# Optimization experiments

Measured on AMD Instinct MI355X. Metric: run time of the kernel, lower is better.

The kernel has to match this reference:

```python
import jax, jax.numpy as jnp
import numpy as np
from jax import lax

# pywt db4 filters. REC_LO is pywt's rec_lo; the others follow pywt's QMF relations:
# rec_hi[k] = (-1)**k * rec_lo[F-1-k]; dec_lo = rec_lo[::-1]; dec_hi = rec_hi[::-1].
REC_LO = np.array([0.23037781330885523, 0.7148465705525415, 0.6308807679295904,
                   -0.027983769416983849, -0.18703481171888114, 0.030841381835986965,
                   0.032883011666982945, -0.010597401784997278], dtype=np.float32)
F = 8
REC_HI = np.array([(-1.0) ** k * REC_LO[F - 1 - k] for k in range(F)], dtype=np.float32)
DEC_LO = REC_LO[::-1].copy()
DEC_HI = REC_HI[::-1].copy()
LEVELS = 3


def _conv(x, kern, stride=1, lhs_dilation=1, padding=((0, 0),)):
    # x: (N, 1, L) ; 1-D correlation (jax conv does NOT flip the kernel)
    k = jnp.asarray(kern, x.dtype).reshape(1, 1, -1)
    return lax.conv_general_dilated(x, k, window_strides=(stride,), padding=padding,
                                    lhs_dilation=(lhs_dilation,),
                                    dimension_numbers=('NCH', 'OIH', 'NCH'))


def dwt(x):
    # pywt single-level dwt, mode='symmetric': extend by F-1 each side, then
    # decimated convolution with dec filters. Equivalent to: drop first extended
    # sample and stride-2 correlate with reversed dec filter (= rec filter).
    xe = jnp.pad(x, ((0, 0), (0, 0), (F - 1, F - 1)), mode='symmetric')[..., 1:]
    cA = _conv(xe, REC_LO, stride=2)   # rev(DEC_LO) == REC_LO
    cD = _conv(xe, REC_HI, stride=2)   # rev(DEC_HI) == REC_HI
    return cA, cD


def idwt(a, d):
    # pywt idwt: upsample by 2 (zeros between samples, len 2L-1), full-convolve
    # with rec filters, trim F-2 from each side -> len 2L - F + 2.
    # Via dilated conv: lhs_dilation=2, pad 1 each side, correlate with rev(rec)=dec.
    ra = _conv(a, DEC_LO, lhs_dilation=2, padding=((1, 1),))
    rd = _conv(d, DEC_HI, lhs_dilation=2, padding=((1, 1),))
    return ra + rd


def waverec(coeffs):
    a = coeffs[0]
    for d in coeffs[1:]:
        if a.shape[-1] == d.shape[-1] + 1:
            a = a[..., :-1]
        a = idwt(a, d)
    return a


def setup_inputs() -> dict:
    key = jax.random.key(0)
    x = jax.random.normal(key, (32, 64, 8192), dtype=jnp.float32)
    return {"x": x}


def reference(x):
    B, C, n = x.shape
    a = x.reshape(B * C, 1, n)
    details = []
    for _ in range(LEVELS):
        a, d = dwt(a)
        details.append(d)
    coeffs = [a] + details[::-1]  # [cA_L, cD_L, ..., cD_1] as in pywt.wavedec
    bands = []
    for i in range(LEVELS + 1):
        kept = [c if j == i else jnp.zeros_like(c) for j, c in enumerate(coeffs)]
        rec = waverec(kept)[..., :n]
        bands.append(rec.reshape(B, C, n))
    return tuple(bands)
```

## Files before the change

kernel.cpp:

```cpp
#include <hip/hip_runtime.h>


#define T      256
#define N0     8192
#define L1     4099
#define L2     2053
#define L3     1030
#define NROWS  2048
#define TW     256
#define WSLICE 960

#define RL0 0.23037781330885523f
#define RL1 0.7148465705525415f
#define RL2 0.6308807679295904f
#define RL3 (-0.02798376941698385f)
#define RL4 (-0.18703481171888114f)
#define RL5 0.030841381835986965f
#define RL6 0.032883011666982945f
#define RL7 (-0.010597401784997278f)

__device__ __forceinline__ int reflect(int m, int n)
{
    m = (m < 0) ? (-1 - m) : m;
    m = (m >= n) ? (2 * n - 1 - m) : m;
    return m;
}

__device__ __forceinline__ void fwd_win(const float* __restrict__ src, int src_lo,
                                        float* __restrict__ dstA, float* __restrict__ dstD,
                                        int out_lo, int out_len, int Lv, int lane)
{
    const float lo[8] = {RL0, RL1, RL2, RL3, RL4, RL5, RL6, RL7};
    const float hi[8] = {RL7, -RL6, RL5, -RL4, RL3, -RL2, RL1, -RL0};
    const float2* s2 = (const float2*)src;
    for (int idx = lane; idx < out_len; idx += 64) {
        int g  = out_lo + idx;
        int ge = reflect(g, Lv);
        int h  = (2 * ge - 6 - src_lo) >> 1;
        float2 p0 = s2[h], p1 = s2[h + 1], p2 = s2[h + 2], p3 = s2[h + 3];
        float w[8] = {p0.x, p0.y, p1.x, p1.y, p2.x, p2.y, p3.x, p3.y};
        float sa = 0.f, sd = 0.f;
#pragma unroll
        for (int k = 0; k < 8; ++k) {
            sa = fmaf(w[k], lo[k], sa);
            sd = fmaf(w[k], hi[k], sd);
        }
        dstA[idx] = sa;
        dstD[idx] = sd;
    }
}

__device__ __forceinline__ void up_win(const float* __restrict__ src, int src_lo,
                                       float* __restrict__ dst, int t0, int pairs,
                                       float o0, float o1, float o2, float o3,
                                       float e0, float e1, float e2, float e3, int lane)
{
    for (int idx = lane; idx < pairs; idx += 64) {
        int b = t0 + idx - src_lo;
        float s0 = src[b], s1 = src[b + 1], s2 = src[b + 2], s3 = src[b + 3];
        float ev = s0 * e0 + s1 * e1 + s2 * e2 + s3 * e3;
        float od = s0 * o0 + s1 * o1 + s2 * o2 + s3 * o3;
        ((float2*)dst)[idx] = make_float2(ev, od);
    }
}

__device__ __forceinline__ void fin_win(const float* __restrict__ src, int src_lo, int w0,
                                        float* __restrict__ g,
                                        float o0, float o1, float o2, float o3,
                                        float e0, float e1, float e2, float e3, int lane)
{
    int b = (w0 >> 1) + 2 * lane - src_lo;
    const float2* s2 = (const float2*)src;
    float2 q0 = s2[b >> 1], q1 = s2[(b >> 1) + 1];
    float s4 = src[b + 4];
    float a0 = q0.x, a1 = q0.y, a2 = q1.x, a3 = q1.y;
    float4 o;
    o.x = a0 * e0 + a1 * e1 + a2 * e2 + a3 * e3;
    o.y = a0 * o0 + a1 * o1 + a2 * o2 + a3 * o3;
    o.z = a1 * e0 + a2 * e1 + a3 * e2 + s4 * e3;
    o.w = a1 * o0 + a2 * o1 + a3 * o2 + s4 * o3;
    ((float4*)(g + w0))[lane] = o;
}


__global__ __launch_bounds__(T) void wavelet_bands(const float* __restrict__ x,
                                                   float* __restrict__ out)
{
    __shared__ float buf[4 * WSLICE];
    const int tid  = threadIdx.x;
    const int lane = tid & 63;
    const int wid  = tid >> 6;
    const int bid  = blockIdx.x;
    const int row  = bid >> 3;
    const int w0   = ((bid & 7) * 4 + wid) * TW;

    float* wbuf = buf + wid * WSLICE;
    float* xw  = wbuf;
    float* a1w = wbuf + 360;
    float* d1w = wbuf + 534;
    float* a2w = wbuf + 708;
    float* d2w = wbuf + 792;
    float* a3w = wbuf + 876;
    float* d3w = wbuf + 915;
    float* t2  = wbuf;
    float* t1a = wbuf + 136;
    float* t1d = wbuf + 208;
    float* t2a = wbuf + 360;
    float* t2d = wbuf + 534;

    const int lo1 = (w0 >> 1) - 18;
    const int lo2 = (w0 >> 2) - 6;
    const int lo3 = (w0 >> 3);
    const int lox = w0 - 48;

    const float* xr = x + (size_t)row * N0;
    const size_t band = (size_t)NROWS * N0;
    float* o0p = out + (size_t)row * N0;
    float* o1p = o0p + band;
    float* o2p = o0p + 2 * band;
    float* o3p = o0p + 3 * band;

    if (w0 == 0 || w0 == N0 - TW) {
        for (int idx = lane; idx < 360; idx += 64)
            xw[idx] = xr[reflect(lox + idx, N0)];
    } else {
        const float4* xr4 = (const float4*)xr;
        float4* xw4 = (float4*)xw;
        const int q0 = lox >> 2;
        for (int i = lane; i < 90; i += 64)
            xw4[i] = xr4[q0 + i];
    }

    fwd_win(xw, lox, a1w, d1w, lo1, TW / 2 + 46, L1, lane);

    fwd_win(a1w, lo1, a2w, d2w, lo2, TW / 4 + 20, L2, lane);
    fin_win(d1w, lo1, w0, o3p, -RL0, -RL2, -RL4, -RL6, RL1, RL3, RL5, RL7, lane);

    fwd_win(a2w, lo2, a3w, d3w, lo3, TW / 8 + 7, L3, lane);
    up_win(d2w, lo2, t2, w0 >> 2, TW / 4 + 2, -RL0, -RL2, -RL4, -RL6, RL1, RL3, RL5, RL7, lane);

    fin_win(t2, w0 >> 1, w0, o2p, RL7, RL5, RL3, RL1, RL6, RL4, RL2, RL0, lane);
    up_win(a3w, lo3, t1a, w0 >> 3, TW / 8 + 3, RL7, RL5, RL3, RL1, RL6, RL4, RL2, RL0, lane);
    up_win(d3w, lo3, t1d, w0 >> 3, TW / 8 + 3, -RL0, -RL2, -RL4, -RL6, RL1, RL3, RL5, RL7, lane);

    up_win(t1a, w0 >> 2, t2a, w0 >> 2, TW / 4 + 2, RL7, RL5, RL3, RL1, RL6, RL4, RL2, RL0, lane);
    up_win(t1d, w0 >> 2, t2d, w0 >> 2, TW / 4 + 2, RL7, RL5, RL3, RL1, RL6, RL4, RL2, RL0, lane);

    fin_win(t2a, w0 >> 1, w0, o0p, RL7, RL5, RL3, RL1, RL6, RL4, RL2, RL0, lane);
    fin_win(t2d, w0 >> 1, w0, o1p, RL7, RL5, RL3, RL1, RL6, RL4, RL2, RL0, lane);
}

extern "C" void kernel_launch(void* const* d_in, const int* in_sizes, int n_in,
                              void* d_out, int out_size, void* d_ws, size_t ws_size,
                              hipStream_t stream)
{
    const float* x = (const float*)d_in[0];
    float* out = (float*)d_out;
    wavelet_bands<<<NROWS * 8, T, 0, stream>>>(x, out);
}
```

Measured before the change: 313.9 us.

## Fuse level-1 DWT into band-3 output and level-2 from global; vectorize upsampling

For interior windows, the level-1 detail band output and the level-2 coefficients are now computed directly from global x with float4 loads, skipping the shared-memory staging of x and the level-1 arrays. The per-pair upsampling helper is replaced by a version that computes two output pairs per lane with float4 stores, and the shared buffer offsets are realigned to 16 bytes. This removes LDS traffic and passes over the data, but recomputes level-1 coefficients redundantly (lvl2_fused computes 8 a1 values per output) and issues more, overlapping global loads per lane.

```diff
diff --git a/kernel.cpp b/kernel.cpp
--- a/kernel.cpp
+++ b/kernel.cpp
@@ -47,20 +47,6 @@
         }
         dstA[idx] = sa;
         dstD[idx] = sd;
-    }
-}
-
-__device__ __forceinline__ void up_win(const float* __restrict__ src, int src_lo,
-                                       float* __restrict__ dst, int t0, int pairs,
-                                       float o0, float o1, float o2, float o3,
-                                       float e0, float e1, float e2, float e3, int lane)
-{
-    for (int idx = lane; idx < pairs; idx += 64) {
-        int b = t0 + idx - src_lo;
-        float s0 = src[b], s1 = src[b + 1], s2 = src[b + 2], s3 = src[b + 3];
-        float ev = s0 * e0 + s1 * e1 + s2 * e2 + s3 * e3;
-        float od = s0 * o0 + s1 * o1 + s2 * o2 + s3 * o3;
-        ((float2*)dst)[idx] = make_float2(ev, od);
     }
 }
 
@@ -82,11 +68,99 @@
     ((float4*)(g + w0))[lane] = o;
 }
 
+__device__ __forceinline__ void up2_win(const float* __restrict__ src, int src_lo,
+                                        float* __restrict__ dst, int t0, int pairs,
+                                        float o0, float o1, float o2, float o3,
+                                        float e0, float e1, float e2, float e3, int lane)
+{
+    const float2* s2 = (const float2*)src;
+    const int half = pairs >> 1;
+    if (lane < half) {
+        const int b = t0 + 2 * lane - src_lo;
+        float2 q0 = s2[b >> 1], q1 = s2[(b >> 1) + 1];
+        float s4 = src[b + 4];
+        float a0 = q0.x, a1 = q0.y, a2 = q1.x, a3 = q1.y;
+        float4 r;
+        r.x = a0 * e0 + a1 * e1 + a2 * e2 + a3 * e3;
+        r.y = a0 * o0 + a1 * o1 + a2 * o2 + a3 * o3;
+        r.z = a1 * e0 + a2 * e1 + a3 * e2 + s4 * e3;
+        r.w = a1 * o0 + a2 * o1 + a3 * o2 + s4 * o3;
+        ((float4*)dst)[lane] = r;
+    } else if ((pairs & 1) && lane == half) {
+        const int p = pairs - 1;
+        const int b = t0 + p - src_lo;
+        float2 q0 = s2[b >> 1], q1 = s2[(b >> 1) + 1];
+        float ev = q0.x * e0 + q0.y * e1 + q1.x * e2 + q1.y * e3;
+        float od = q0.x * o0 + q0.y * o1 + q1.x * o2 + q1.y * o3;
+        ((float2*)dst)[p] = make_float2(ev, od);
+    }
+}
+
+__device__ __forceinline__ void o3_fused(const float* __restrict__ xr, int w0,
+                                         float* __restrict__ o3p, int lane)
+{
+    const float hi[8] = {RL7, -RL6, RL5, -RL4, RL3, -RL2, RL1, -RL0};
+    const float4* x4 = (const float4*)xr;
+    const int q0 = (w0 + 4 * lane - 8) >> 2;
+    float f[20];
+#pragma unroll
+    for (int q = 0; q < 5; ++q)
+        *(float4*)&f[4 * q] = x4[q0 + q];
+    float dm[5];
+#pragma unroll
+    for (int j = 0; j < 5; ++j) {
+        float s = 0.f;
+#pragma unroll
+        for (int t = 0; t < 8; ++t) s = fmaf(f[2 + 2 * j + t], hi[t], s);
+        dm[j] = s;
+    }
+    const float e0 = RL1, e1 = RL3, e2 = RL5, e3 = RL7;
+    const float p0 = -RL0, p1 = -RL2, p2 = -RL4, p3 = -RL6;
+    float4 r;
+    r.x = dm[0] * e0 + dm[1] * e1 + dm[2] * e2 + dm[3] * e3;
+    r.y = dm[0] * p0 + dm[1] * p1 + dm[2] * p2 + dm[3] * p3;
+    r.z = dm[1] * e0 + dm[2] * e1 + dm[3] * e2 + dm[4] * e3;
+    r.w = dm[1] * p0 + dm[2] * p1 + dm[3] * p2 + dm[4] * p3;
+    ((float4*)(o3p + w0))[lane] = r;
+}
+
+__device__ __forceinline__ void lvl2_fused(const float* __restrict__ xr, int lo2,
+                                           float* __restrict__ a2w,
+                                           float* __restrict__ d2w, int lane)
+{
+    const float lo[8] = {RL0, RL1, RL2, RL3, RL4, RL5, RL6, RL7};
+    const float hi[8] = {RL7, -RL6, RL5, -RL4, RL3, -RL2, RL1, -RL0};
+    const float4* x4 = (const float4*)xr;
+    for (int idx = lane; idx < 84; idx += 64) {
+        const int i  = lo2 + idx;
+        const int q0 = i - 5;
+        float f[24];
+#pragma unroll
+        for (int q = 0; q < 6; ++q)
+            *(float4*)&f[4 * q] = x4[q0 + q];
+        float a1v[8];
+#pragma unroll
+        for (int k = 0; k < 8; ++k) {
+            float s = 0.f;
+#pragma unroll
+            for (int j = 0; j < 8; ++j) s = fmaf(f[2 + 2 * k + j], lo[j], s);
+            a1v[k] = s;
+        }
+        float sa = 0.f, sd = 0.f;
+#pragma unroll
+        for (int k = 0; k < 8; ++k) {
+            sa = fmaf(a1v[k], lo[k], sa);
+            sd = fmaf(a1v[k], hi[k], sd);
+        }
+        a2w[idx] = sa;
+        d2w[idx] = sd;
+    }
+}
 
 __global__ __launch_bounds__(T) void wavelet_bands(const float* __restrict__ x,
                                                    float* __restrict__ out)
 {
-    __shared__ float buf[4 * WSLICE];
+    __shared__ __align__(16) float buf[4 * WSLICE];
     const int tid  = threadIdx.x;
     const int lane = tid & 63;
     const int wid  = tid >> 6;
@@ -101,12 +175,12 @@
     float* a2w = wbuf + 708;
     float* d2w = wbuf + 792;
     float* a3w = wbuf + 876;
-    float* d3w = wbuf + 915;
+    float* d3w = wbuf + 916;
     float* t2  = wbuf;
     float* t1a = wbuf + 136;
     float* t1d = wbuf + 208;
     float* t2a = wbuf + 360;
-    float* t2d = wbuf + 534;
+    float* t2d = wbuf + 536;
 
     const int lo1 = (w0 >> 1) - 18;
     const int lo2 = (w0 >> 2) - 6;
@@ -123,28 +197,23 @@
     if (w0 == 0 || w0 == N0 - TW) {
         for (int idx = lane; idx < 360; idx += 64)
             xw[idx] = xr[reflect(lox + idx, N0)];
+        fwd_win(xw, lox, a1w, d1w, lo1, TW / 2 + 46, L1, lane);
+        fwd_win(a1w, lo1, a2w, d2w, lo2, TW / 4 + 20, L2, lane);
+        fin_win(d1w, lo1, w0, o3p, -RL0, -RL2, -RL4, -RL6, RL1, RL3, RL5, RL7, lane);
     } else {
-        const float4* xr4 = (const float4*)xr;
-        float4* xw4 = (float4*)xw;
-        const int q0 = lox >> 2;
-        for (int i = lane; i < 90; i += 64)
-            xw4[i] = xr4[q0 + i];
-    }
-
-    fwd_win(xw, lox, a1w, d1w, lo1, TW / 2 + 46, L1, lane);
-
-    fwd_win(a1w, lo1, a2w, d2w, lo2, TW / 4 + 20, L2, lane);
-    fin_win(d1w, lo1, w0, o3p, -RL0, -RL2, -RL4, -RL6, RL1, RL3, RL5, RL7, lane);
+        o3_fused(xr, w0, o3p, lane);
+        lvl2_fused(xr, lo2, a2w, d2w, lane);
+    }
 
     fwd_win(a2w, lo2, a3w, d3w, lo3, TW / 8 + 7, L3, lane);
-    up_win(d2w, lo2, t2, w0 >> 2, TW / 4 + 2, -RL0, -RL2, -RL4, -RL6, RL1, RL3, RL5, RL7, lane);
+    up2_win(d2w, lo2, t2, w0 >> 2, TW / 4 + 2, -RL0, -RL2, -RL4, -RL6, RL1, RL3, RL5, RL7, lane);
 
     fin_win(t2, w0 >> 1, w0, o2p, RL7, RL5, RL3, RL1, RL6, RL4, RL2, RL0, lane);
-    up_win(a3w, lo3, t1a, w0 >> 3, TW / 8 + 3, RL7, RL5, RL3, RL1, RL6, RL4, RL2, RL0, lane);
-    up_win(d3w, lo3, t1d, w0 >> 3, TW / 8 + 3, -RL0, -RL2, -RL4, -RL6, RL1, RL3, RL5, RL7, lane);
-
-    up_win(t1a, w0 >> 2, t2a, w0 >> 2, TW / 4 + 2, RL7, RL5, RL3, RL1, RL6, RL4, RL2, RL0, lane);
-    up_win(t1d, w0 >> 2, t2d, w0 >> 2, TW / 4 + 2, RL7, RL5, RL3, RL1, RL6, RL4, RL2, RL0, lane);
+    up2_win(a3w, lo3, t1a, w0 >> 3, TW / 8 + 3, RL7, RL5, RL3, RL1, RL6, RL4, RL2, RL0, lane);
+    up2_win(d3w, lo3, t1d, w0 >> 3, TW / 8 + 3, -RL0, -RL2, -RL4, -RL6, RL1, RL3, RL5, RL7, lane);
+
+    up2_win(t1a, w0 >> 2, t2a, w0 >> 2, TW / 4 + 2, RL7, RL5, RL3, RL1, RL6, RL4, RL2, RL0, lane);
+    up2_win(t1d, w0 >> 2, t2d, w0 >> 2, TW / 4 + 2, RL7, RL5, RL3, RL1, RL6, RL4, RL2, RL0, lane);
 
     fin_win(t2a, w0 >> 1, w0, o0p, RL7, RL5, RL3, RL1, RL6, RL4, RL2, RL0, lane);
     fin_win(t2d, w0 >> 1, w0, o1p, RL7, RL5, RL3, RL1, RL6, RL4, RL2, RL0, lane);
```

Result: slower. 332.6 us (+6.0%).
